# Performance work log

Hardware: AMD Instinct MI355X
Metric: run time of the kernel (lower is better)

## Reference

```python
import jax, jax.numpy as jnp
import numpy as np

ITERS = 3

def squash(s, axis):
    # v = (|s|^2 / (1 + |s|^2)) * s / |s|
    sn = jnp.sum(s * s, axis=axis, keepdims=True)
    return sn / (1.0 + sn) * s / jnp.sqrt(sn)

def setup_inputs() -> dict:
    key = jax.random.key(0)
    k1, k2 = jax.random.split(key)
    b, B, C, P2, f = 8, 144, 16, 16, 12
    u = jax.random.normal(k1, (b, B, C, P2, f, f), dtype=jnp.float32)
    a = jax.random.uniform(k2, (b, B, f, f), dtype=jnp.float32)
    return {"u": u, "a": a}

def reference(u, a):
    # u: (b, B, C, P2, f, f); a: (b, B, f, f)
    b, B, C, P2, f, _ = u.shape
    # r: (b, B, C, 1, f, f), initialized uniform over C scaled by activation
    r = jnp.broadcast_to(a[:, :, None, None, :, :] * (1.0 / C), (b, B, C, 1, f, f))
    v = None
    for i in range(ITERS):
        c = jax.nn.softmax(r, axis=2)                       # over C
        v = squash(jnp.sum(c * u, axis=1, keepdims=True), axis=3)  # (b,1,C,P2,f,f)
        if i != ITERS - 1:
            r = r + jnp.sum(u * v, axis=3, keepdims=True)   # agreement over psize
    a_out = jnp.sqrt(jnp.sum(v * v, axis=3, keepdims=True))  # (b,1,C,1,f,f)
    return (jnp.squeeze(v, axis=1), jnp.squeeze(a_out, axis=(1, 3)))
```

## Files before the change

### kernel.cpp

```cpp
#include <hip/hip_runtime.h>
#include <math.h>


#define NB 8
#define BDIM 144
#define CDIM 16
#define PDIM 16
#define SDIM 144
#define PT 16
#define BC 8
#define NPT (SDIM / PT)
#define NBC (BDIM / BC)
#define USTRIDE (CDIM * PDIM * SDIM)
#define VELEMS (NB * CDIM * PDIM * SDIM)
#define AELEMS (NB * CDIM * SDIM)

__global__ __launch_bounds__(256) void s_kernel(const float* __restrict__ u,
                                                const float* __restrict__ a,
                                                const float* __restrict__ V,
                                                float* __restrict__ s,
                                                int iter) {
  __shared__ float Vt[CDIM][PDIM][PT];
  __shared__ float ebuf[2][CDIM][PT + 1];
  __shared__ float atile[BC][PT];

  const int tid = threadIdx.x;
  const int pos = tid & 15;
  const int c = tid >> 4;
  const int b = blockIdx.z;
  const int posg = blockIdx.y * PT + pos;
  const int B0 = blockIdx.x * BC;

  const float* ubase =
      u + ((size_t)((b * BDIM + B0) * CDIM + c) * PDIM) * SDIM + posg;

  float sacc[PDIM];
#pragma unroll
  for (int p = 0; p < PDIM; ++p) sacc[p] = 0.f;

  if (iter == 0) {
#pragma unroll 2
    for (int j = 0; j < BC; ++j) {
      const float* ub = ubase + (size_t)j * USTRIDE;
#pragma unroll
      for (int p = 0; p < PDIM; ++p) sacc[p] += ub[p * SDIM];
    }
    const int sb = ((b * CDIM + c) * PDIM) * SDIM + posg;
#pragma unroll
    for (int p = 0; p < PDIM; ++p)
      atomicAdd(&s[sb + p * SDIM], sacc[p] * (1.0f / CDIM));
    return;
  }

  {
    const int vb = ((b * CDIM + c) * PDIM) * SDIM + posg;
#pragma unroll
    for (int p = 0; p < PDIM; ++p) Vt[c][p][pos] = V[vb + p * SDIM];
    if (tid < BC * PT) {
      const int j = tid >> 4;
      atile[j][pos] =
          a[(b * BDIM + B0 + j) * SDIM + blockIdx.y * PT + pos] * (1.0f / CDIM);
    }
  }
  __syncthreads();

  float uvbuf[2][PDIM];
#pragma unroll
  for (int p = 0; p < PDIM; ++p) uvbuf[0][p] = ubase[p * SDIM];

#pragma unroll
  for (int j = 0; j < BC; ++j) {
    float* uv = uvbuf[j & 1];
    float* uvn = uvbuf[(j + 1) & 1];
    if (j + 1 < BC) {
      const float* ub = ubase + (size_t)(j + 1) * USTRIDE;
#pragma unroll
      for (int p = 0; p < PDIM; ++p) uvn[p] = ub[p * SDIM];
    }
    float dot = 0.f;
#pragma unroll
    for (int p = 0; p < PDIM; ++p) dot += uv[p] * Vt[c][p][pos];
    const float e = __expf(atile[j][pos] + dot);
    ebuf[j & 1][c][pos] = e;
    __syncthreads();
    float sum = 0.f;
#pragma unroll
    for (int c2 = 0; c2 < CDIM; ++c2) sum += ebuf[j & 1][c2][pos];
    const float w = e * __builtin_amdgcn_rcpf(sum);
#pragma unroll
    for (int p = 0; p < PDIM; ++p) sacc[p] += w * uv[p];
  }

  const int sb = ((b * CDIM + c) * PDIM) * SDIM + posg;
#pragma unroll
  for (int p = 0; p < PDIM; ++p) atomicAdd(&s[sb + p * SDIM], sacc[p]);
}

__global__ __launch_bounds__(256) void q_kernel(float* __restrict__ s,
                                                float* __restrict__ V,
                                                float* __restrict__ out_v,
                                                float* __restrict__ out_a,
                                                int iter) {
  const int gid = blockIdx.x * 256 + threadIdx.x;
  const int b = gid / (CDIM * SDIM);
  const int rem = gid - b * (CDIM * SDIM);
  const int c = rem / SDIM;
  const int posg = rem - c * SDIM;
  const int base = ((b * CDIM + c) * PDIM) * SDIM + posg;

  float sv[PDIM];
  float sn = 0.f;
#pragma unroll
  for (int p = 0; p < PDIM; ++p) {
    const float x = s[base + p * SDIM];
    sv[p] = x;
    sn += x * x;
  }
  const float scale = sn / (1.0f + sn) * rsqrtf(sn);

  if (iter < 2) {
#pragma unroll
    for (int p = 0; p < PDIM; ++p) {
      V[base + p * SDIM] += sv[p] * scale;
      s[base + p * SDIM] = 0.f;
    }
  } else {
    float vv = 0.f;
#pragma unroll
    for (int p = 0; p < PDIM; ++p) {
      const float v = sv[p] * scale;
      out_v[base + p * SDIM] = v;
      vv += v * v;
    }
    out_a[gid] = sqrtf(vv);
  }
}

extern "C" void kernel_launch(void* const* d_in, const int* in_sizes, int n_in,
                              void* d_out, int out_size, void* d_ws, size_t ws_size,
                              hipStream_t stream) {
  const float* u = (const float*)d_in[0];
  const float* a = (const float*)d_in[1];
  float* V = (float*)d_ws;
  float* s = V + VELEMS;
  float* out_v = (float*)d_out;
  float* out_a = out_v + VELEMS;

  hipMemsetAsync(d_ws, 0, (size_t)2 * VELEMS * sizeof(float), stream);

  const dim3 gS(NBC, NPT, NB);
  for (int it = 0; it < 3; ++it) {
    s_kernel<<<gS, 256, 0, stream>>>(u, a, V, s, it);
    q_kernel<<<AELEMS / 256, 256, 0, stream>>>(s, V, out_v, out_a, it);
  }
}
```

Before: 355.3 us.

## Replace atomics with per-chunk partial sums and vectorize with wave-shuffle softmax

Each s-pass block now writes its partial sums for one B-chunk into a separate slab instead of using atomicAdd, and a new reduction kernel sums the slabs. Each thread now handles four positions through float4 loads, and the softmax over C uses wave shuffles instead of shared memory and __syncthreads. The initial memset is removed because V is written directly on iteration 0. The cost is an extra reduction kernel per iteration and a large partial buffer of 18×VELEMS floats that must be written and read back.

```diff
diff --git a/kernel.cpp b/kernel.cpp
--- a/kernel.cpp
+++ b/kernel.cpp
@@ -7,132 +7,185 @@
 #define CDIM 16
 #define PDIM 16
 #define SDIM 144
-#define PT 16
 #define BC 8
-#define NPT (SDIM / PT)
 #define NBC (BDIM / BC)
-#define USTRIDE (CDIM * PDIM * SDIM)
+#define NPT 9
 #define VELEMS (NB * CDIM * PDIM * SDIM)
 #define AELEMS (NB * CDIM * SDIM)
-
-__global__ __launch_bounds__(256) void s_kernel(const float* __restrict__ u,
-                                                const float* __restrict__ a,
-                                                const float* __restrict__ V,
-                                                float* __restrict__ s,
-                                                int iter) {
-  __shared__ float Vt[CDIM][PDIM][PT];
-  __shared__ float ebuf[2][CDIM][PT + 1];
-  __shared__ float atile[BC][PT];
-
+#define USTRIDE (CDIM * PDIM * SDIM)
+
+__device__ __forceinline__ float4 ld4(const float* p) { return *(const float4*)p; }
+__device__ __forceinline__ void st4(float* p, float4 v) { *(float4*)p = v; }
+
+__global__ __launch_bounds__(64) void s_pass0(const float* __restrict__ u,
+                                              float* __restrict__ s_part) {
   const int tid = threadIdx.x;
-  const int pos = tid & 15;
-  const int c = tid >> 4;
+  const int posq = tid & 3;
+  const int c = tid >> 2;
   const int b = blockIdx.z;
-  const int posg = blockIdx.y * PT + pos;
+  const int pos0 = blockIdx.y * 16 + posq * 4;
+  const float* ubase =
+      u + (size_t)((b * BDIM + blockIdx.x * BC) * CDIM + c) * (PDIM * SDIM) + pos0;
+
+  float4 sacc[PDIM];
+#pragma unroll
+  for (int p = 0; p < PDIM; ++p) sacc[p] = make_float4(0.f, 0.f, 0.f, 0.f);
+
+#pragma unroll 1
+  for (int j = 0; j < BC; ++j) {
+    const float* ub = ubase + (size_t)j * USTRIDE;
+#pragma unroll
+    for (int p = 0; p < PDIM; ++p) {
+      const float4 uv = ld4(ub + p * SDIM);
+      sacc[p].x += uv.x; sacc[p].y += uv.y; sacc[p].z += uv.z; sacc[p].w += uv.w;
+    }
+  }
+  float* sp = s_part + (size_t)blockIdx.x * VELEMS +
+              (size_t)((b * CDIM + c) * PDIM) * SDIM + pos0;
+#pragma unroll
+  for (int p = 0; p < PDIM; ++p) {
+    float4 o;
+    o.x = sacc[p].x * 0.0625f; o.y = sacc[p].y * 0.0625f;
+    o.z = sacc[p].z * 0.0625f; o.w = sacc[p].w * 0.0625f;
+    st4(sp + p * SDIM, o);
+  }
+}
+
+__global__ __launch_bounds__(64) void s_pass(const float* __restrict__ u,
+                                             const float* __restrict__ a,
+                                             const float* __restrict__ V,
+                                             float* __restrict__ s_part) {
+  const int tid = threadIdx.x;
+  const int posq = tid & 3;
+  const int c = tid >> 2;
+  const int b = blockIdx.z;
+  const int pos0 = blockIdx.y * 16 + posq * 4;
   const int B0 = blockIdx.x * BC;
-
   const float* ubase =
-      u + ((size_t)((b * BDIM + B0) * CDIM + c) * PDIM) * SDIM + posg;
-
-  float sacc[PDIM];
-#pragma unroll
-  for (int p = 0; p < PDIM; ++p) sacc[p] = 0.f;
-
-  if (iter == 0) {
-#pragma unroll 2
-    for (int j = 0; j < BC; ++j) {
-      const float* ub = ubase + (size_t)j * USTRIDE;
-#pragma unroll
-      for (int p = 0; p < PDIM; ++p) sacc[p] += ub[p * SDIM];
-    }
-    const int sb = ((b * CDIM + c) * PDIM) * SDIM + posg;
-#pragma unroll
-    for (int p = 0; p < PDIM; ++p)
-      atomicAdd(&s[sb + p * SDIM], sacc[p] * (1.0f / CDIM));
-    return;
-  }
-
+      u + (size_t)((b * BDIM + B0) * CDIM + c) * (PDIM * SDIM) + pos0;
+
+  float4 Vt[PDIM];
   {
-    const int vb = ((b * CDIM + c) * PDIM) * SDIM + posg;
-#pragma unroll
-    for (int p = 0; p < PDIM; ++p) Vt[c][p][pos] = V[vb + p * SDIM];
-    if (tid < BC * PT) {
-      const int j = tid >> 4;
-      atile[j][pos] =
-          a[(b * BDIM + B0 + j) * SDIM + blockIdx.y * PT + pos] * (1.0f / CDIM);
-    }
-  }
-  __syncthreads();
-
-  float uvbuf[2][PDIM];
-#pragma unroll
-  for (int p = 0; p < PDIM; ++p) uvbuf[0][p] = ubase[p * SDIM];
-
-#pragma unroll
+    const float* vb = V + (size_t)((b * CDIM + c) * PDIM) * SDIM + pos0;
+#pragma unroll
+    for (int p = 0; p < PDIM; ++p) Vt[p] = ld4(vb + p * SDIM);
+  }
+
+  float4 sacc[PDIM];
+#pragma unroll
+  for (int p = 0; p < PDIM; ++p) sacc[p] = make_float4(0.f, 0.f, 0.f, 0.f);
+
+#pragma unroll 1
   for (int j = 0; j < BC; ++j) {
-    float* uv = uvbuf[j & 1];
-    float* uvn = uvbuf[(j + 1) & 1];
-    if (j + 1 < BC) {
-      const float* ub = ubase + (size_t)(j + 1) * USTRIDE;
-#pragma unroll
-      for (int p = 0; p < PDIM; ++p) uvn[p] = ub[p * SDIM];
-    }
-    float dot = 0.f;
-#pragma unroll
-    for (int p = 0; p < PDIM; ++p) dot += uv[p] * Vt[c][p][pos];
-    const float e = __expf(atile[j][pos] + dot);
-    ebuf[j & 1][c][pos] = e;
-    __syncthreads();
-    float sum = 0.f;
-#pragma unroll
-    for (int c2 = 0; c2 < CDIM; ++c2) sum += ebuf[j & 1][c2][pos];
-    const float w = e * __builtin_amdgcn_rcpf(sum);
-#pragma unroll
-    for (int p = 0; p < PDIM; ++p) sacc[p] += w * uv[p];
-  }
-
-  const int sb = ((b * CDIM + c) * PDIM) * SDIM + posg;
-#pragma unroll
-  for (int p = 0; p < PDIM; ++p) atomicAdd(&s[sb + p * SDIM], sacc[p]);
-}
-
-__global__ __launch_bounds__(256) void q_kernel(float* __restrict__ s,
-                                                float* __restrict__ V,
-                                                float* __restrict__ out_v,
-                                                float* __restrict__ out_a,
-                                                int iter) {
+    const float* ub = ubase + (size_t)j * USTRIDE;
+    float4 uv[PDIM];
+#pragma unroll
+    for (int p = 0; p < PDIM; ++p) uv[p] = ld4(ub + p * SDIM);
+
+    float4 dotv = make_float4(0.f, 0.f, 0.f, 0.f);
+#pragma unroll
+    for (int p = 0; p < PDIM; ++p) {
+      dotv.x += uv[p].x * Vt[p].x; dotv.y += uv[p].y * Vt[p].y;
+      dotv.z += uv[p].z * Vt[p].z; dotv.w += uv[p].w * Vt[p].w;
+    }
+    const float4 a4 = ld4(a + (size_t)(b * BDIM + B0 + j) * SDIM + pos0);
+    float4 e;
+    e.x = __expf(a4.x * 0.0625f + dotv.x);
+    e.y = __expf(a4.y * 0.0625f + dotv.y);
+    e.z = __expf(a4.z * 0.0625f + dotv.z);
+    e.w = __expf(a4.w * 0.0625f + dotv.w);
+    float4 ssum = e;
+#pragma unroll
+    for (int m = 4; m <= 32; m <<= 1) {
+      ssum.x += __shfl_xor(ssum.x, m);
+      ssum.y += __shfl_xor(ssum.y, m);
+      ssum.z += __shfl_xor(ssum.z, m);
+      ssum.w += __shfl_xor(ssum.w, m);
+    }
+    float4 w;
+    w.x = e.x * __builtin_amdgcn_rcpf(ssum.x);
+    w.y = e.y * __builtin_amdgcn_rcpf(ssum.y);
+    w.z = e.z * __builtin_amdgcn_rcpf(ssum.z);
+    w.w = e.w * __builtin_amdgcn_rcpf(ssum.w);
+#pragma unroll
+    for (int p = 0; p < PDIM; ++p) {
+      sacc[p].x += w.x * uv[p].x; sacc[p].y += w.y * uv[p].y;
+      sacc[p].z += w.z * uv[p].z; sacc[p].w += w.w * uv[p].w;
+    }
+  }
+
+  float* sp = s_part + (size_t)blockIdx.x * VELEMS +
+              (size_t)((b * CDIM + c) * PDIM) * SDIM + pos0;
+#pragma unroll
+  for (int p = 0; p < PDIM; ++p) st4(sp + p * SDIM, sacc[p]);
+}
+
+__global__ __launch_bounds__(256) void s_red_k(const float* __restrict__ s_part,
+                                               float* __restrict__ s_red) {
   const int gid = blockIdx.x * 256 + threadIdx.x;
-  const int b = gid / (CDIM * SDIM);
-  const int rem = gid - b * (CDIM * SDIM);
-  const int c = rem / SDIM;
-  const int posg = rem - c * SDIM;
-  const int base = ((b * CDIM + c) * PDIM) * SDIM + posg;
-
-  float sv[PDIM];
-  float sn = 0.f;
+  const float4* sp = (const float4*)s_part;
+  float4 acc = sp[gid];
+#pragma unroll 1
+  for (int ch = 1; ch < NBC; ++ch) {
+    const float4 x = sp[(size_t)ch * (VELEMS / 4) + gid];
+    acc.x += x.x; acc.y += x.y; acc.z += x.z; acc.w += x.w;
+  }
+  ((float4*)s_red)[gid] = acc;
+}
+
+__global__ __launch_bounds__(64) void q_kernel(const float* __restrict__ s_red,
+                                               float* __restrict__ V,
+                                               float* __restrict__ out_v,
+                                               float* __restrict__ out_a,
+                                               int iter) {
+  const int gid = blockIdx.x * 64 + threadIdx.x;
+  const int posq = gid % (SDIM / 4);
+  const int rem = gid / (SDIM / 4);
+  const int c = rem & 15;
+  const int b = rem >> 4;
+  const int pos0 = posq * 4;
+  const size_t base = (size_t)((b * CDIM + c) * PDIM) * SDIM + pos0;
+
+  float4 sv[PDIM];
+  float4 sn = make_float4(0.f, 0.f, 0.f, 0.f);
 #pragma unroll
   for (int p = 0; p < PDIM; ++p) {
-    const float x = s[base + p * SDIM];
-    sv[p] = x;
-    sn += x * x;
-  }
-  const float scale = sn / (1.0f + sn) * rsqrtf(sn);
+    sv[p] = ld4(s_red + base + p * SDIM);
+    sn.x += sv[p].x * sv[p].x; sn.y += sv[p].y * sv[p].y;
+    sn.z += sv[p].z * sv[p].z; sn.w += sv[p].w * sv[p].w;
+  }
+  float4 g;
+  g.x = sn.x * __builtin_amdgcn_rcpf(1.f + sn.x);
+  g.y = sn.y * __builtin_amdgcn_rcpf(1.f + sn.y);
+  g.z = sn.z * __builtin_amdgcn_rcpf(1.f + sn.z);
+  g.w = sn.w * __builtin_amdgcn_rcpf(1.f + sn.w);
+  float4 sc;
+  sc.x = g.x * rsqrtf(sn.x); sc.y = g.y * rsqrtf(sn.y);
+  sc.z = g.z * rsqrtf(sn.z); sc.w = g.w * rsqrtf(sn.w);
 
   if (iter < 2) {
 #pragma unroll
     for (int p = 0; p < PDIM; ++p) {
-      V[base + p * SDIM] += sv[p] * scale;
-      s[base + p * SDIM] = 0.f;
+      float4 nv;
+      nv.x = sv[p].x * sc.x; nv.y = sv[p].y * sc.y;
+      nv.z = sv[p].z * sc.z; nv.w = sv[p].w * sc.w;
+      if (iter == 0) {
+        st4(V + base + p * SDIM, nv);
+      } else {
+        float4 ov = ld4(V + base + p * SDIM);
+        ov.x += nv.x; ov.y += nv.y; ov.z += nv.z; ov.w += nv.w;
+        st4(V + base + p * SDIM, ov);
+      }
     }
   } else {
-    float vv = 0.f;
-#pragma unroll
-    for (int p = 0; p < PDIM; ++p) {
-      const float v = sv[p] * scale;
-      out_v[base + p * SDIM] = v;
-      vv += v * v;
-    }
-    out_a[gid] = sqrtf(vv);
+#pragma unroll
+    for (int p = 0; p < PDIM; ++p) {
+      float4 nv;
+      nv.x = sv[p].x * sc.x; nv.y = sv[p].y * sc.y;
+      nv.z = sv[p].z * sc.z; nv.w = sv[p].w * sc.w;
+      st4(out_v + base + p * SDIM, nv);
+    }
+    st4(out_a + (size_t)(b * CDIM + c) * SDIM + pos0, g);
   }
 }
 
@@ -142,15 +195,24 @@
   const float* u = (const float*)d_in[0];
   const float* a = (const float*)d_in[1];
   float* V = (float*)d_ws;
-  float* s = V + VELEMS;
+  float* s_red = V + VELEMS;
+  float* s_part = s_red + VELEMS;
   float* out_v = (float*)d_out;
   float* out_a = out_v + VELEMS;
 
-  hipMemsetAsync(d_ws, 0, (size_t)2 * VELEMS * sizeof(float), stream);
-
   const dim3 gS(NBC, NPT, NB);
-  for (int it = 0; it < 3; ++it) {
-    s_kernel<<<gS, 256, 0, stream>>>(u, a, V, s, it);
-    q_kernel<<<AELEMS / 256, 256, 0, stream>>>(s, V, out_v, out_a, it);
-  }
-}
+  const int gR = VELEMS / 4 / 256;
+  const int gQ = AELEMS / 4 / 64;
+
+  s_pass0<<<gS, 64, 0, stream>>>(u, s_part);
+  s_red_k<<<gR, 256, 0, stream>>>(s_part, s_red);
+  q_kernel<<<gQ, 64, 0, stream>>>(s_red, V, out_v, out_a, 0);
+
+  s_pass<<<gS, 64, 0, stream>>>(u, a, V, s_part);
+  s_red_k<<<gR, 256, 0, stream>>>(s_part, s_red);
+  q_kernel<<<gQ, 64, 0, stream>>>(s_red, V, out_v, out_a, 1);
+
+  s_pass<<<gS, 64, 0, stream>>>(u, a, V, s_part);
+  s_red_k<<<gR, 256, 0, stream>>>(s_part, s_red);
+  q_kernel<<<gQ, 64, 0, stream>>>(s_red, V, out_v, out_a, 2);
+}
```

New measurement: 379.8 us. 6.9% more time.
